# Optimization experiments

Hardware: AMD Instinct MI355X
Metric: run time of the kernel (lower is better)

## Reference

```python
import jax, jax.numpy as jnp
import numpy as np

EMB = 1024
FF = 4096
NE = 8
TOPK = 2
TEMP = 1.0


def setup_inputs() -> dict:
    key = jax.random.key(0)
    ks = jax.random.split(key, 8)
    s_emb = 1.0 / np.sqrt(EMB)
    s_ff = 1.0 / np.sqrt(FF)
    x = jax.random.normal(ks[0], (4, 2048, EMB), dtype=jnp.float32)
    gate_W = jax.random.uniform(ks[1], (EMB, NE), minval=-s_emb, maxval=s_emb, dtype=jnp.float32)
    gate_b = jax.random.uniform(ks[2], (NE,), minval=-s_emb, maxval=s_emb, dtype=jnp.float32)
    W1 = jax.random.uniform(ks[3], (NE, EMB, FF), minval=-s_emb, maxval=s_emb, dtype=jnp.float32)
    b1 = jax.random.uniform(ks[4], (NE, FF), minval=-s_emb, maxval=s_emb, dtype=jnp.float32)
    W2 = jax.random.uniform(ks[5], (NE, FF, EMB), minval=-s_ff, maxval=s_ff, dtype=jnp.float32)
    b2 = jax.random.uniform(ks[6], (NE, EMB), minval=-s_ff, maxval=s_ff, dtype=jnp.float32)
    return {"x": x, "gate_W": gate_W, "gate_b": gate_b, "W1": W1, "b1": b1, "W2": W2, "b2": b2}


def reference(x, gate_W, gate_b, W1, b1, W2, b2):
    B, S, D = x.shape
    xf = x.reshape(-1, D)  # [T, D]
    T = xf.shape[0]

    gate_logits = (xf @ gate_W + gate_b) / TEMP            # [T, E]
    gate_scores = jax.nn.softmax(gate_logits, axis=-1)     # [T, E]
    topk_scores, topk_idx = jax.lax.top_k(gate_scores, TOPK)
    topk_scores = topk_scores / jnp.sum(topk_scores, axis=-1, keepdims=True)

    # combine_weights[t, e] = sum_i topk_scores[t, i] * (topk_idx[t, i] == e)
    onehot = jax.nn.one_hot(topk_idx, NE, dtype=xf.dtype)  # [T, K, E]
    combine = jnp.einsum('tk,tke->te', topk_scores, onehot)  # [T, E]

    # Dense per-expert FFN (dropout is identity in eval): h = gelu(x W1 + b1); y = h W2 + b2
    h = jax.nn.gelu(jnp.einsum('td,edf->etf', xf, W1) + b1[:, None, :], approximate=False)
    y = jnp.einsum('etf,efd->etd', h, W2) + b2[:, None, :]  # [E, T, D]
    out = jnp.einsum('te,etd->td', combine, y).reshape(B, S, D)

    # Load-balance auxiliary loss
    expert_counts = jnp.sum(onehot, axis=(0, 1))            # [E]
    expert_fraction = expert_counts / (T * TOPK)
    routing_weights = jnp.mean(gate_scores, axis=0)
    aux_loss = NE * jnp.sum(expert_fraction * routing_weights)
    return out, aux_loss
```

## Files before the change

### kernel.cpp

```cpp
#include <hip/hip_runtime.h>
#include <math.h>

#define EMB 1024
#define FF  4096
#define NE  8
#define TTOK 8192

typedef __attribute__((ext_vector_type(4))) float  f32x4;
typedef __attribute__((ext_vector_type(8))) __bf16 bf16x8;
typedef __attribute__((ext_vector_type(4))) __bf16 bf16x4;

#define MAXROWS  18432

#define WS_COUNTS  0
#define WS_CURSORS 1024
#define WS_SSUM    1056
#define WS_NTILES  2080
#define WS_BASE    2084
#define WS_TILE_E  2176
#define WS_TILE_RB 2816
#define WS_TKIDX   4096
#define WS_TKW     69632
#define WS_SLOT    135168
#define WS_TOKID   200704
#define WS_ROWW    274432
#define WS_BIG2    350208

#define SZ_W1T ((size_t)NE * EMB * FF * 2)
#define SZ_W2T ((size_t)NE * EMB * FF * 2)
#define SZ_XB  ((size_t)TTOK * EMB * 2)
#define SZ_H   ((size_t)MAXROWS * FF * 2)
#define SZ_XG  ((size_t)MAXROWS * EMB * 2)
#define SZ_Y2  ((size_t)MAXROWS * EMB * 2)

__device__ inline f32x4 fzero() { f32x4 v = {0.f, 0.f, 0.f, 0.f}; return v; }

__device__ __forceinline__ void gl16(const void* g, void* l) {
    __builtin_amdgcn_global_load_lds(
        (const __attribute__((address_space(1))) void*)g,
        (__attribute__((address_space(3))) void*)l, 16, 0, 0);
}

#define DSR(dst, addr, off) \
    asm volatile("ds_read_b128 %0, %1 offset:" #off : "=v"(dst) : "v"(addr))

__device__ __forceinline__ float gelu_f(float v) {
    float u = fabsf(v) * 0.70710678118654752f;
    float p = 1.0f + u * (0.278393f + u * (0.230389f + u * (0.000972f + u * 0.078108f)));
    p = p * p; p = p * p;
    float er = 1.0f - 1.0f / p;
    float s = (v >= 0.0f) ? er : -er;
    return 0.5f * v * (1.0f + s);
}

__global__ __launch_bounds__(256) void gate_kernel(
    const float* __restrict__ x, const float* __restrict__ gW, const float* __restrict__ gb,
    int* counts, float* ssum, int* tk_idx, float* tk_w, __bf16* __restrict__ xb)
{
    int wave = threadIdx.x >> 6;
    int lane = threadIdx.x & 63;
    int t = blockIdx.x * 4 + wave;

    float acc[NE];
#pragma unroll
    for (int e = 0; e < NE; e++) acc[e] = 0.f;

    const float* xr = x + (size_t)t * EMB;
    __bf16* xbr = xb + (size_t)t * EMB;
#pragma unroll
    for (int i = 0; i < 4; i++) {
        int d0 = i * 256 + lane * 4;
        f32x4 xv = *(const f32x4*)(xr + d0);
        bf16x4 cv;
#pragma unroll
        for (int q = 0; q < 4; q++) cv[q] = (__bf16)xv[q];
        *(bf16x4*)(xbr + d0) = cv;
#pragma unroll
        for (int j = 0; j < 4; j++) {
            const float* wrow = gW + (size_t)(d0 + j) * NE;
            float xs = xv[j];
#pragma unroll
            for (int e = 0; e < NE; e++) acc[e] += xs * wrow[e];
        }
    }
#pragma unroll
    for (int e = 0; e < NE; e++) {
#pragma unroll
        for (int off = 32; off; off >>= 1) acc[e] += __shfl_xor(acc[e], off, 64);
    }
    if (lane == 0) {
        float sc[NE];
        float m = -1e30f;
        for (int e = 0; e < NE; e++) { sc[e] = acc[e] + gb[e]; m = fmaxf(m, sc[e]); }
        float sum = 0.f;
        for (int e = 0; e < NE; e++) { sc[e] = expf(sc[e] - m); sum += sc[e]; }
        float inv = 1.f / sum;
        for (int e = 0; e < NE; e++) sc[e] *= inv;
        int i0 = 0; float s0 = sc[0];
        for (int e = 1; e < NE; e++) if (sc[e] > s0) { s0 = sc[e]; i0 = e; }
        int i1 = -1; float s1 = -1e30f;
        for (int e = 0; e < NE; e++) if (e != i0 && sc[e] > s1) { s1 = sc[e]; i1 = e; }
        float rn = 1.f / (s0 + s1);
        tk_idx[2 * t]     = i0;  tk_idx[2 * t + 1] = i1;
        tk_w[2 * t]       = s0 * rn;  tk_w[2 * t + 1] = s1 * rn;
        int slot = blockIdx.x & 31;
        atomicAdd(&counts[i0 * 32 + slot], 1);
        atomicAdd(&counts[i1 * 32 + slot], 1);
        for (int e = 0; e < NE; e++) atomicAdd(&ssum[e * 32 + slot], sc[e]);
    }
}

__global__ void route_build_kernel(const int* counts, const float* ssum,
                                   int* ntiles, int* base, int* tile_e, int* tile_rb,
                                   float* out_aux)
{
    if (threadIdx.x != 0 || blockIdx.x != 0) return;
    int total = 0, tiles = 0;
    float aux = 0.f;
    for (int e = 0; e < NE; e++) {
        int c = 0; float ss = 0.f;
        for (int j = 0; j < 32; j++) { c += counts[e * 32 + j]; ss += ssum[e * 32 + j]; }
        base[e] = total;
        int nt = (c + 255) >> 8;
        for (int i = 0; i < nt; i++) { tile_e[tiles] = e; tile_rb[tiles] = total + (i << 8); tiles++; }
        total += nt << 8;
        aux += ((float)c / (float)(TTOK * 2)) * (ss / (float)TTOK);
    }
    *ntiles = tiles;
    *out_aux = aux * (float)NE;
}

__global__ __launch_bounds__(256) void scatter_kernel(
    const int* __restrict__ tk_idx, const float* __restrict__ tk_w,
    const int* __restrict__ base, int* cursors, int* token_id, float* roww,
    int* slot_of)
{
    int t = blockIdx.x * 256 + threadIdx.x;
#pragma unroll
    for (int k = 0; k < 2; k++) {
        int e = tk_idx[2 * t + k];
        int pos = atomicAdd(&cursors[e], 1);
        int slot = base[e] + pos;
        token_id[slot] = t;
        roww[slot] = tk_w[2 * t + k];
        slot_of[2 * t + k] = slot;
    }
}

__global__ __launch_bounds__(256) void pack_x_kernel(
    const __bf16* __restrict__ xb, const int* __restrict__ token_id,
    __bf16* __restrict__ xg)
{
    int tid = threadIdx.x;
    int slot = blockIdx.x * 2 + (tid >> 7);
    int off = (tid & 127) * 8;
    int tok = token_id[slot];
    uint4 v = {0u, 0u, 0u, 0u};
    if (tok >= 0) v = *(const uint4*)(xb + (size_t)tok * EMB + off);
    *(uint4*)(xg + (size_t)slot * EMB + off) = v;
}

__global__ __launch_bounds__(256) void combine_kernel(
    const __bf16* __restrict__ y0, const __bf16* __restrict__ y1, int nsplit,
    const int* __restrict__ slot_of,
    const int* __restrict__ tk_idx, const float* __restrict__ tk_w,
    const float* __restrict__ b2, float* __restrict__ out)
{
    int t = blockIdx.x;
    int dq = threadIdx.x * 4;
    int s0 = slot_of[2 * t], s1 = slot_of[2 * t + 1];
    int e0 = tk_idx[2 * t], e1 = tk_idx[2 * t + 1];
    float w0 = tk_w[2 * t], w1 = tk_w[2 * t + 1];
    bf16x4 va = *(const bf16x4*)(y0 + (size_t)s0 * EMB + dq);
    bf16x4 vb = *(const bf16x4*)(y0 + (size_t)s1 * EMB + dq);
    f32x4 ya, yb;
#pragma unroll
    for (int q = 0; q < 4; q++) { ya[q] = (float)va[q]; yb[q] = (float)vb[q]; }
    if (nsplit == 2) {
        bf16x4 za = *(const bf16x4*)(y1 + (size_t)s0 * EMB + dq);
        bf16x4 zb = *(const bf16x4*)(y1 + (size_t)s1 * EMB + dq);
#pragma unroll
        for (int q = 0; q < 4; q++) { ya[q] += (float)za[q]; yb[q] += (float)zb[q]; }
    }
    f32x4 ba = *(const f32x4*)(b2 + (size_t)e0 * EMB + dq);
    f32x4 bb = *(const f32x4*)(b2 + (size_t)e1 * EMB + dq);
    f32x4 r;
#pragma unroll
    for (int q = 0; q < 4; q++) r[q] = w0 * (ya[q] + ba[q]) + w1 * (yb[q] + bb[q]);
    *(f32x4*)(out + (size_t)t * EMB + dq) = r;
}

__global__ __launch_bounds__(256) void transpose_cvt2_kernel(
    const float* __restrict__ W1, __bf16* __restrict__ W1T,
    const float* __restrict__ W2, __bf16* __restrict__ W2T)
{
    int f = blockIdx.x;
    int which = f >> 13; f &= 8191;
    int e = f >> 10; f &= 1023;
    int R, C, bx, by;
    const float* src; __bf16* dst;
    if (which == 0) { R = EMB; C = FF;  bx = f & 15; by = f >> 4; src = W1; dst = W1T; }
    else            { R = FF;  C = EMB; bx = f & 63; by = f >> 6; src = W2; dst = W2T; }
    src += (size_t)e * R * C;
    dst += (size_t)e * R * C;
    __shared__ __bf16 Ls[64 * 72];
    int t = threadIdx.x;
    int r0 = bx * 64, c0 = by * 64;
    int ri = t >> 4, cj = (t & 15) * 4;
#pragma unroll
    for (int p = 0; p < 4; p++) {
        int r = ri + p * 16;
        f32x4 v = *(const f32x4*)(src + (size_t)(r0 + r) * C + c0 + cj);
#pragma unroll
        for (int q = 0; q < 4; q++) Ls[(cj + q) * 72 + r] = (__bf16)v[q];
    }
    __syncthreads();
    int c = t >> 2, rq = (t & 3) * 16;
    bf16x8 a = *(bf16x8*)&Ls[c * 72 + rq];
    bf16x8 b = *(bf16x8*)&Ls[c * 72 + rq + 8];
    *(bf16x8*)(dst + (size_t)(c0 + c) * R + r0 + rq) = a;
    *(bf16x8*)(dst + (size_t)(c0 + c) * R + r0 + rq + 8) = b;
}


template <bool PACKED>
__global__ __launch_bounds__(512, 2) void gemm1_8p(
    const __bf16* __restrict__ xsrc, const __bf16* __restrict__ W1T,
    const float* __restrict__ b1,
    const int* __restrict__ token_id, const int* __restrict__ tile_e,
    const int* __restrict__ tile_rb, const int* __restrict__ ntiles,
    __bf16* __restrict__ h)
{
    extern __shared__ __bf16 lds[];
    int flat = blockIdx.x;
    int c8 = flat & 7, r = flat >> 3;
    int mti = r >> 4, nb = r & 15;
    int mt = c8 * 9 + mti;
    if (mt >= *ntiles) return;
    int e = tile_e[mt], rb = tile_rb[mt];
    int n0 = nb * 256;

    int tid = threadIdx.x, lane = tid & 63, wid = tid >> 6;
    int wr = wid >> 2, wc = wid & 3;
    int cl = lane & 15, cq = lane >> 4;

    int srow = tid >> 2;
    int schunk = (tid & 3) ^ ((tid >> 3) & 3);
    const __bf16* ag[2];
#pragma unroll
    for (int hm = 0; hm < 2; hm++) {
        if (PACKED) {
            ag[hm] = xsrc + (size_t)(rb + hm * 128 + srow) * EMB + schunk * 8;
        } else {
            int tok = token_id[rb + hm * 128 + srow];
            if (tok < 0) tok = 0;
            ag[hm] = xsrc + (size_t)tok * EMB + schunk * 8;
        }
    }
    const __bf16* bg[2];
#pragma unroll
    for (int hn = 0; hn < 2; hn++)
        bg[hn] = W1T + ((size_t)e * FF + (size_t)(n0 + hn * 128 + srow)) * EMB + schunk * 8;

    int sdA0 = wid * 512, sdA1 = 4096 + wid * 512;
    int sdB0 = 8192 + wid * 512, sdB1 = 12288 + wid * 512;

    uint32_t lb = (uint32_t)(uintptr_t)(__attribute__((address_space(3))) __bf16*)lds;
    int xoffe = (cq ^ ((cl >> 1) & 3)) * 8;
    uint32_t ab0 = lb + 2u * (uint32_t)(wr * 4096 + cl * 32 + xoffe);
    uint32_t bb0 = lb + 2u * (uint32_t)(8192 + (wc >> 1) * 4096 + ((wc & 1) * 64 + cl) * 32 + xoffe);

    f32x4 acc[8][4];
#pragma unroll
    for (int i = 0; i < 8; i++)
#pragma unroll
        for (int j = 0; j < 4; j++) acc[i][j] = fzero();

    const int NT = EMB / 32;
#pragma unroll
    for (int t0 = 0; t0 < 3; t0++) {
        __bf16* bp = lds + t0 * 16384;
        int k0 = t0 * 32;
        gl16(ag[0] + k0, bp + sdA0);
        gl16(ag[1] + k0, bp + sdA1);
        gl16(bg[0] + k0, bp + sdB0);
        gl16(bg[1] + k0, bp + sdB1);
    }
    asm volatile("s_waitcnt vmcnt(8)" ::: "memory");
    __builtin_amdgcn_s_barrier();

#pragma unroll 1
    for (int t = 0; t < NT; t++) {
        uint32_t cboff = (uint32_t)(t & 3) * 32768u;
        uint32_t aaddr = ab0 + cboff, baddr = bb0 + cboff;
        bf16x8 b[4], a[8];
        DSR(b[0], baddr, 0);    DSR(b[1], baddr, 1024);
        DSR(b[2], baddr, 2048); DSR(b[3], baddr, 3072);
        DSR(a[0], aaddr, 0);    DSR(a[1], aaddr, 1024);
        DSR(a[2], aaddr, 2048); DSR(a[3], aaddr, 3072);
        DSR(a[4], aaddr, 4096); DSR(a[5], aaddr, 5120);
        DSR(a[6], aaddr, 6144); DSR(a[7], aaddr, 7168);

        int kt = t + 3;
        if (kt < NT) {
            __bf16* sp = lds + (kt & 3) * 16384;
            int ko = kt * 32;
            gl16(ag[0] + ko, sp + sdA0);
            gl16(ag[1] + ko, sp + sdA1);
            gl16(bg[0] + ko, sp + sdB0);
            gl16(bg[1] + ko, sp + sdB1);
        }

        asm volatile("s_waitcnt lgkmcnt(0)" ::: "memory");
        __builtin_amdgcn_sched_barrier(0);
        __builtin_amdgcn_s_setprio(1);
#pragma unroll
        for (int mi = 0; mi < 8; mi++)
#pragma unroll
            for (int ni = 0; ni < 4; ni++)
                acc[mi][ni] = __builtin_amdgcn_mfma_f32_16x16x32_bf16(a[mi], b[ni], acc[mi][ni], 0, 0, 0);
        __builtin_amdgcn_s_setprio(0);

        if (t < NT - 3)       { asm volatile("s_waitcnt vmcnt(8)" ::: "memory"); }
        else if (t == NT - 3) { asm volatile("s_waitcnt vmcnt(4)" ::: "memory"); }
        else if (t == NT - 2) { asm volatile("s_waitcnt vmcnt(0)" ::: "memory"); }
        if (t < NT - 1) __builtin_amdgcn_s_barrier();
    }

    const float* b1g = b1 + (size_t)e * FF + n0;
#pragma unroll
    for (int mi = 0; mi < 8; mi++) {
#pragma unroll
        for (int ni = 0; ni < 4; ni++) {
            int col = wc * 64 + ni * 16 + cl;
            float bias = b1g[col];
#pragma unroll
            for (int j = 0; j < 4; j++) {
                int row = wr * 128 + mi * 16 + cq * 4 + j;
                float v = acc[mi][ni][j] + bias;
                h[(size_t)(rb + row) * FF + n0 + col] = (__bf16)gelu_f(v);
            }
        }
    }
}

__global__ __launch_bounds__(512, 2) void gemm2_8p(
    const __bf16* __restrict__ h, const __bf16* __restrict__ W2T,
    const int* __restrict__ tile_e, const int* __restrict__ tile_rb,
    const int* __restrict__ ntiles,
    __bf16* __restrict__ y0, __bf16* __restrict__ y1, int nsplit)
{
    extern __shared__ __bf16 lds[];
    int flat = blockIdx.x;
    int c8 = flat & 7, r = flat >> 3;
    int z = r / 36; int r36 = r - z * 36;
    int mti = r36 >> 2, nb = r36 & 3;
    int mt = c8 * 9 + mti;
    if (mt >= *ntiles) return;
    int e = tile_e[mt], rb = tile_rb[mt];
    int n0 = nb * 256;
    int KC = FF / nsplit;
    int koff = z * KC;
    __bf16* y = z ? y1 : y0;

    int tid = threadIdx.x, lane = tid & 63, wid = tid >> 6;
    int wr = wid >> 2, wc = wid & 3;
    int cl = lane & 15, cq = lane >> 4;

    int srow = tid >> 2;
    int schunk = (tid & 3) ^ ((tid >> 3) & 3);
    const __bf16* ag[2];
#pragma unroll
    for (int hm = 0; hm < 2; hm++)
        ag[hm] = h + (size_t)(rb + hm * 128 + srow) * FF + koff + schunk * 8;
    const __bf16* bg[2];
#pragma unroll
    for (int hn = 0; hn < 2; hn++)
        bg[hn] = W2T + ((size_t)e * EMB + (size_t)(n0 + hn * 128 + srow)) * FF + koff + schunk * 8;

    int sdA0 = wid * 512, sdA1 = 4096 + wid * 512;
    int sdB0 = 8192 + wid * 512, sdB1 = 12288 + wid * 512;

    uint32_t lb = (uint32_t)(uintptr_t)(__attribute__((address_space(3))) __bf16*)lds;
    int xoffe = (cq ^ ((cl >> 1) & 3)) * 8;
    uint32_t ab0 = lb + 2u * (uint32_t)(wr * 4096 + cl * 32 + xoffe);
    uint32_t bb0 = lb + 2u * (uint32_t)(8192 + (wc >> 1) * 4096 + ((wc & 1) * 64 + cl) * 32 + xoffe);

    f32x4 acc[8][4];
#pragma unroll
    for (int i = 0; i < 8; i++)
#pragma unroll
        for (int j = 0; j < 4; j++) acc[i][j] = fzero();

    const int NT = KC / 32;
#pragma unroll
    for (int t0 = 0; t0 < 3; t0++) {
        __bf16* bp = lds + t0 * 16384;
        int k0 = t0 * 32;
        gl16(ag[0] + k0, bp + sdA0);
        gl16(ag[1] + k0, bp + sdA1);
        gl16(bg[0] + k0, bp + sdB0);
        gl16(bg[1] + k0, bp + sdB1);
    }
    asm volatile("s_waitcnt vmcnt(8)" ::: "memory");
    __builtin_amdgcn_s_barrier();

#pragma unroll 1
    for (int t = 0; t < NT; t++) {
        uint32_t cboff = (uint32_t)(t & 3) * 32768u;
        uint32_t aaddr = ab0 + cboff, baddr = bb0 + cboff;
        bf16x8 b[4], a[8];
        DSR(b[0], baddr, 0);    DSR(b[1], baddr, 1024);
        DSR(b[2], baddr, 2048); DSR(b[3], baddr, 3072);
        DSR(a[0], aaddr, 0);    DSR(a[1], aaddr, 1024);
        DSR(a[2], aaddr, 2048); DSR(a[3], aaddr, 3072);
        DSR(a[4], aaddr, 4096); DSR(a[5], aaddr, 5120);
        DSR(a[6], aaddr, 6144); DSR(a[7], aaddr, 7168);

        int kt = t + 3;
        if (kt < NT) {
            __bf16* sp = lds + (kt & 3) * 16384;
            int ko = kt * 32;
            gl16(ag[0] + ko, sp + sdA0);
            gl16(ag[1] + ko, sp + sdA1);
            gl16(bg[0] + ko, sp + sdB0);
            gl16(bg[1] + ko, sp + sdB1);
        }

        asm volatile("s_waitcnt lgkmcnt(0)" ::: "memory");
        __builtin_amdgcn_sched_barrier(0);
        __builtin_amdgcn_s_setprio(1);
#pragma unroll
        for (int mi = 0; mi < 8; mi++)
#pragma unroll
            for (int ni = 0; ni < 4; ni++)
                acc[mi][ni] = __builtin_amdgcn_mfma_f32_16x16x32_bf16(a[mi], b[ni], acc[mi][ni], 0, 0, 0);
        __builtin_amdgcn_s_setprio(0);

        if (t < NT - 3)       { asm volatile("s_waitcnt vmcnt(8)" ::: "memory"); }
        else if (t == NT - 3) { asm volatile("s_waitcnt vmcnt(4)" ::: "memory"); }
        else if (t == NT - 2) { asm volatile("s_waitcnt vmcnt(0)" ::: "memory"); }
        if (t < NT - 1) __builtin_amdgcn_s_barrier();
    }

#pragma unroll
    for (int mi = 0; mi < 8; mi++) {
#pragma unroll
        for (int ni = 0; ni < 4; ni++) {
            int col = wc * 64 + ni * 16 + cl;
#pragma unroll
            for (int j = 0; j < 4; j++) {
                int row = wr * 128 + mi * 16 + cq * 4 + j;
                y[(size_t)(rb + row) * EMB + n0 + col] = (__bf16)acc[mi][ni][j];
            }
        }
    }
}

extern "C" void kernel_launch(void* const* d_in, const int* in_sizes, int n_in,
                              void* d_out, int out_size, void* d_ws, size_t ws_size,
                              hipStream_t stream)
{
    const float* x   = (const float*)d_in[0];
    const float* gW  = (const float*)d_in[1];
    const float* gb  = (const float*)d_in[2];
    const float* W1  = (const float*)d_in[3];
    const float* b1  = (const float*)d_in[4];
    const float* W2  = (const float*)d_in[5];
    const float* b2  = (const float*)d_in[6];
    float* out = (float*)d_out;

    char* ws = (char*)d_ws;
    int*   counts  = (int*)(ws + WS_COUNTS);
    int*   cursors = (int*)(ws + WS_CURSORS);
    float* ssum    = (float*)(ws + WS_SSUM);
    int*   ntiles  = (int*)(ws + WS_NTILES);
    int*   base    = (int*)(ws + WS_BASE);
    int*   tile_e  = (int*)(ws + WS_TILE_E);
    int*   tile_rb = (int*)(ws + WS_TILE_RB);
    int*   tk_idx  = (int*)(ws + WS_TKIDX);
    float* tk_w    = (float*)(ws + WS_TKW);
    int*   slot_of = (int*)(ws + WS_SLOT);
    int*   token_id= (int*)(ws + WS_TOKID);
    float* roww    = (float*)(ws + WS_ROWW);

    __bf16* W1T  = (__bf16*)(ws + WS_BIG2);
    __bf16* xb   = (__bf16*)(ws + WS_BIG2 + SZ_W1T);
    __bf16* W2T  = (__bf16*)(ws + WS_BIG2 + SZ_W1T + SZ_XB);
    __bf16* hbuf = (__bf16*)(ws + WS_BIG2 + SZ_W1T + SZ_XB + SZ_W2T);
    size_t fixedend = WS_BIG2 + SZ_W1T + SZ_XB + SZ_W2T;

    __bf16* y0 = (__bf16*)(ws + WS_BIG2);
    __bf16* xg = (__bf16*)(ws + fixedend + SZ_H);
    bool packed = (ws_size >= fixedend + SZ_H + SZ_XG);
    __bf16* y1 = (__bf16*)(ws + fixedend + SZ_H + (packed ? SZ_XG : 0));
    int nsplit = (ws_size >= fixedend + SZ_H + (packed ? SZ_XG : 0) + SZ_Y2) ? 2 : 1;

    hipFuncSetAttribute((const void*)gemm1_8p<true>,  hipFuncAttributeMaxDynamicSharedMemorySize, 131072);
    hipFuncSetAttribute((const void*)gemm1_8p<false>, hipFuncAttributeMaxDynamicSharedMemorySize, 131072);
    hipFuncSetAttribute((const void*)gemm2_8p, hipFuncAttributeMaxDynamicSharedMemorySize, 131072);

    hipMemsetAsync(ws + WS_COUNTS, 0, 2080, stream);
    hipMemsetAsync(ws + WS_TOKID, 0xFF, (size_t)MAXROWS * 4, stream);

    transpose_cvt2_kernel<<<16384, 256, 0, stream>>>(W1, W1T, W2, W2T);

    gate_kernel<<<TTOK / 4, 256, 0, stream>>>(x, gW, gb, counts, ssum, tk_idx, tk_w, xb);
    route_build_kernel<<<1, 64, 0, stream>>>(counts, ssum, ntiles, base, tile_e, tile_rb,
                                             out + (size_t)TTOK * EMB);
    scatter_kernel<<<TTOK / 256, 256, 0, stream>>>(tk_idx, tk_w, base, cursors, token_id, roww, slot_of);

    if (packed) {
        pack_x_kernel<<<MAXROWS / 2, 256, 0, stream>>>(xb, token_id, xg);
        gemm1_8p<true><<<8 * 9 * 16, 512, 131072, stream>>>(
            xg, W1T, b1, token_id, tile_e, tile_rb, ntiles, hbuf);
    } else {
        gemm1_8p<false><<<8 * 9 * 16, 512, 131072, stream>>>(
            xb, W1T, b1, token_id, tile_e, tile_rb, ntiles, hbuf);
    }
    gemm2_8p<<<8 * 9 * 4 * nsplit, 512, 131072, stream>>>(
        hbuf, W2T, tile_e, tile_rb, ntiles, y0, y1, nsplit);
    combine_kernel<<<TTOK, 256, 0, stream>>>(y0, y1, nsplit, slot_of, tk_idx, tk_w, b2, out);
}
```

Before: 685.5 us.

## Shrink expert GEMM tiles to 128x128 with 256 threads and triple buffering

Both grouped expert GEMMs move from 256x256 output tiles (512 threads, 4-stage LDS ring, 128KB) to 128x128 tiles (256 threads, 3-stage ring, 48KB), with three blocks per CU. The grid grows fourfold, which improves load balance and wave filling across the CUs and gives more resident blocks to hide latency. In exchange, each block reuses its operands less, so global and L2 traffic per FLOP roughly doubles, and the prefetch depth drops from three stages to two.

```diff
diff --git a/kernel.cpp b/kernel.cpp
--- a/kernel.cpp
+++ b/kernel.cpp
@@ -224,7 +224,7 @@
 
 
 template <bool PACKED>
-__global__ __launch_bounds__(512, 2) void gemm1_8p(
+__global__ __launch_bounds__(256, 3) void gemm1_8p(
     const __bf16* __restrict__ xsrc, const __bf16* __restrict__ W1T,
     const float* __restrict__ b1,
     const int* __restrict__ token_id, const int* __restrict__ tile_e,
@@ -234,25 +234,27 @@
     extern __shared__ __bf16 lds[];
     int flat = blockIdx.x;
     int c8 = flat & 7, r = flat >> 3;
-    int mti = r >> 4, nb = r & 15;
-    int mt = c8 * 9 + mti;
-    if (mt >= *ntiles) return;
-    int e = tile_e[mt], rb = tile_rb[mt];
-    int n0 = nb * 256;
+    int sti = r >> 5, nb = r & 31;
+    int st = c8 * 18 + sti;
+    if (st >= *ntiles * 2) return;
+    int e = tile_e[st >> 1];
+    int rb = tile_rb[st >> 1] + (st & 1) * 128;
+    int n0 = nb * 128;
 
     int tid = threadIdx.x, lane = tid & 63, wid = tid >> 6;
-    int wr = wid >> 2, wc = wid & 3;
+    int wr = wid >> 1, wc = wid & 1;
     int cl = lane & 15, cq = lane >> 4;
 
-    int srow = tid >> 2;
+    int srow1 = ((tid >> 6) << 4) | ((tid & 63) >> 2);
     int schunk = (tid & 3) ^ ((tid >> 3) & 3);
     const __bf16* ag[2];
 #pragma unroll
     for (int hm = 0; hm < 2; hm++) {
+        int row = srow1 + hm * 64;
         if (PACKED) {
-            ag[hm] = xsrc + (size_t)(rb + hm * 128 + srow) * EMB + schunk * 8;
+            ag[hm] = xsrc + (size_t)(rb + row) * EMB + schunk * 8;
         } else {
-            int tok = token_id[rb + hm * 128 + srow];
+            int tok = token_id[rb + row];
             if (tok < 0) tok = 0;
             ag[hm] = xsrc + (size_t)tok * EMB + schunk * 8;
         }
@@ -260,50 +262,50 @@
     const __bf16* bg[2];
 #pragma unroll
     for (int hn = 0; hn < 2; hn++)
-        bg[hn] = W1T + ((size_t)e * FF + (size_t)(n0 + hn * 128 + srow)) * EMB + schunk * 8;
-
-    int sdA0 = wid * 512, sdA1 = 4096 + wid * 512;
-    int sdB0 = 8192 + wid * 512, sdB1 = 12288 + wid * 512;
+        bg[hn] = W1T + ((size_t)e * FF + (size_t)(n0 + srow1 + hn * 64)) * EMB + schunk * 8;
+
+    int sdA0 = wid * 512, sdA1 = 2048 + wid * 512;
+    int sdB0 = 4096 + wid * 512, sdB1 = 6144 + wid * 512;
 
     uint32_t lb = (uint32_t)(uintptr_t)(__attribute__((address_space(3))) __bf16*)lds;
     int xoffe = (cq ^ ((cl >> 1) & 3)) * 8;
-    uint32_t ab0 = lb + 2u * (uint32_t)(wr * 4096 + cl * 32 + xoffe);
-    uint32_t bb0 = lb + 2u * (uint32_t)(8192 + (wc >> 1) * 4096 + ((wc & 1) * 64 + cl) * 32 + xoffe);
-
-    f32x4 acc[8][4];
-#pragma unroll
-    for (int i = 0; i < 8; i++)
+    uint32_t ab0 = lb + 2u * (uint32_t)(wr * 2048 + cl * 32 + xoffe);
+    uint32_t bb0 = lb + 2u * (uint32_t)(4096 + wc * 2048 + cl * 32 + xoffe);
+
+    f32x4 acc[4][4];
+#pragma unroll
+    for (int i = 0; i < 4; i++)
 #pragma unroll
         for (int j = 0; j < 4; j++) acc[i][j] = fzero();
 
     const int NT = EMB / 32;
 #pragma unroll
-    for (int t0 = 0; t0 < 3; t0++) {
-        __bf16* bp = lds + t0 * 16384;
+    for (int t0 = 0; t0 < 2; t0++) {
+        __bf16* bp = lds + t0 * 8192;
         int k0 = t0 * 32;
         gl16(ag[0] + k0, bp + sdA0);
         gl16(ag[1] + k0, bp + sdA1);
         gl16(bg[0] + k0, bp + sdB0);
         gl16(bg[1] + k0, bp + sdB1);
     }
-    asm volatile("s_waitcnt vmcnt(8)" ::: "memory");
+    asm volatile("s_waitcnt vmcnt(4)" ::: "memory");
     __builtin_amdgcn_s_barrier();
 
+    int cb = 0;
 #pragma unroll 1
     for (int t = 0; t < NT; t++) {
-        uint32_t cboff = (uint32_t)(t & 3) * 32768u;
+        uint32_t cboff = (uint32_t)cb * 16384u;
         uint32_t aaddr = ab0 + cboff, baddr = bb0 + cboff;
-        bf16x8 b[4], a[8];
+        bf16x8 b[4], a[4];
         DSR(b[0], baddr, 0);    DSR(b[1], baddr, 1024);
         DSR(b[2], baddr, 2048); DSR(b[3], baddr, 3072);
         DSR(a[0], aaddr, 0);    DSR(a[1], aaddr, 1024);
         DSR(a[2], aaddr, 2048); DSR(a[3], aaddr, 3072);
-        DSR(a[4], aaddr, 4096); DSR(a[5], aaddr, 5120);
-        DSR(a[6], aaddr, 6144); DSR(a[7], aaddr, 7168);
-
-        int kt = t + 3;
+
+        int kt = t + 2;
         if (kt < NT) {
-            __bf16* sp = lds + (kt & 3) * 16384;
+            int sb = cb + 2; if (sb >= 3) sb -= 3;
+            __bf16* sp = lds + sb * 8192;
             int ko = kt * 32;
             gl16(ag[0] + ko, sp + sdA0);
             gl16(ag[1] + ko, sp + sdA1);
@@ -315,28 +317,28 @@
         __builtin_amdgcn_sched_barrier(0);
         __builtin_amdgcn_s_setprio(1);
 #pragma unroll
-        for (int mi = 0; mi < 8; mi++)
+        for (int mi = 0; mi < 4; mi++)
 #pragma unroll
             for (int ni = 0; ni < 4; ni++)
                 acc[mi][ni] = __builtin_amdgcn_mfma_f32_16x16x32_bf16(a[mi], b[ni], acc[mi][ni], 0, 0, 0);
         __builtin_amdgcn_s_setprio(0);
 
-        if (t < NT - 3)       { asm volatile("s_waitcnt vmcnt(8)" ::: "memory"); }
-        else if (t == NT - 3) { asm volatile("s_waitcnt vmcnt(4)" ::: "memory"); }
+        if (t < NT - 2)       { asm volatile("s_waitcnt vmcnt(4)" ::: "memory"); }
         else if (t == NT - 2) { asm volatile("s_waitcnt vmcnt(0)" ::: "memory"); }
         if (t < NT - 1) __builtin_amdgcn_s_barrier();
+        cb = cb + 1; if (cb >= 3) cb = 0;
     }
 
     const float* b1g = b1 + (size_t)e * FF + n0;
 #pragma unroll
-    for (int mi = 0; mi < 8; mi++) {
+    for (int mi = 0; mi < 4; mi++) {
 #pragma unroll
         for (int ni = 0; ni < 4; ni++) {
             int col = wc * 64 + ni * 16 + cl;
             float bias = b1g[col];
 #pragma unroll
             for (int j = 0; j < 4; j++) {
-                int row = wr * 128 + mi * 16 + cq * 4 + j;
+                int row = wr * 64 + mi * 16 + cq * 4 + j;
                 float v = acc[mi][ni][j] + bias;
                 h[(size_t)(rb + row) * FF + n0 + col] = (__bf16)gelu_f(v);
             }
@@ -344,7 +346,7 @@
     }
 }
 
-__global__ __launch_bounds__(512, 2) void gemm2_8p(
+__global__ __launch_bounds__(256, 3) void gemm2_8p(
     const __bf16* __restrict__ h, const __bf16* __restrict__ W2T,
     const int* __restrict__ tile_e, const int* __restrict__ tile_rb,
     const int* __restrict__ ntiles,
@@ -353,73 +355,74 @@
     extern __shared__ __bf16 lds[];
     int flat = blockIdx.x;
     int c8 = flat & 7, r = flat >> 3;
-    int z = r / 36; int r36 = r - z * 36;
-    int mti = r36 >> 2, nb = r36 & 3;
-    int mt = c8 * 9 + mti;
-    if (mt >= *ntiles) return;
-    int e = tile_e[mt], rb = tile_rb[mt];
-    int n0 = nb * 256;
+    int z = r / 144; int r144 = r - z * 144;
+    int sti = r144 >> 3, nb = r144 & 7;
+    int st = c8 * 18 + sti;
+    if (st >= *ntiles * 2) return;
+    int e = tile_e[st >> 1];
+    int rb = tile_rb[st >> 1] + (st & 1) * 128;
+    int n0 = nb * 128;
     int KC = FF / nsplit;
     int koff = z * KC;
     __bf16* y = z ? y1 : y0;
 
     int tid = threadIdx.x, lane = tid & 63, wid = tid >> 6;
-    int wr = wid >> 2, wc = wid & 3;
+    int wr = wid >> 1, wc = wid & 1;
     int cl = lane & 15, cq = lane >> 4;
 
-    int srow = tid >> 2;
+    int srow1 = ((tid >> 6) << 4) | ((tid & 63) >> 2);
     int schunk = (tid & 3) ^ ((tid >> 3) & 3);
     const __bf16* ag[2];
 #pragma unroll
     for (int hm = 0; hm < 2; hm++)
-        ag[hm] = h + (size_t)(rb + hm * 128 + srow) * FF + koff + schunk * 8;
+        ag[hm] = h + (size_t)(rb + srow1 + hm * 64) * FF + koff + schunk * 8;
     const __bf16* bg[2];
 #pragma unroll
     for (int hn = 0; hn < 2; hn++)
-        bg[hn] = W2T + ((size_t)e * EMB + (size_t)(n0 + hn * 128 + srow)) * FF + koff + schunk * 8;
-
-    int sdA0 = wid * 512, sdA1 = 4096 + wid * 512;
-    int sdB0 = 8192 + wid * 512, sdB1 = 12288 + wid * 512;
+        bg[hn] = W2T + ((size_t)e * EMB + (size_t)(n0 + srow1 + hn * 64)) * FF + koff + schunk * 8;
+
+    int sdA0 = wid * 512, sdA1 = 2048 + wid * 512;
+    int sdB0 = 4096 + wid * 512, sdB1 = 6144 + wid * 512;
 
     uint32_t lb = (uint32_t)(uintptr_t)(__attribute__((address_space(3))) __bf16*)lds;
     int xoffe = (cq ^ ((cl >> 1) & 3)) * 8;
-    uint32_t ab0 = lb + 2u * (uint32_t)(wr * 4096 + cl * 32 + xoffe);
-    uint32_t bb0 = lb + 2u * (uint32_t)(8192 + (wc >> 1) * 4096 + ((wc & 1) * 64 + cl) * 32 + xoffe);
-
-    f32x4 acc[8][4];
-#pragma unroll
-    for (int i = 0; i < 8; i++)
+    uint32_t ab0 = lb + 2u * (uint32_t)(wr * 2048 + cl * 32 + xoffe);
+    uint32_t bb0 = lb + 2u * (uint32_t)(4096 + wc * 2048 + cl * 32 + xoffe);
+
+    f32x4 acc[4][4];
+#pragma unroll
+    for (int i = 0; i < 4; i++)
 #pragma unroll
         for (int j = 0; j < 4; j++) acc[i][j] = fzero();
 
     const int NT = KC / 32;
 #pragma unroll
-    for (int t0 = 0; t0 < 3; t0++) {
-        __bf16* bp = lds + t0 * 16384;
+    for (int t0 = 0; t0 < 2; t0++) {
+        __bf16* bp = lds + t0 * 8192;
         int k0 = t0 * 32;
         gl16(ag[0] + k0, bp + sdA0);
         gl16(ag[1] + k0, bp + sdA1);
         gl16(bg[0] + k0, bp + sdB0);
         gl16(bg[1] + k0, bp + sdB1);
     }
-    asm volatile("s_waitcnt vmcnt(8)" ::: "memory");
+    asm volatile("s_waitcnt vmcnt(4)" ::: "memory");
     __builtin_amdgcn_s_barrier();
 
+    int cb = 0;
 #pragma unroll 1
     for (int t = 0; t < NT; t++) {
-        uint32_t cboff = (uint32_t)(t & 3) * 32768u;
+        uint32_t cboff = (uint32_t)cb * 16384u;
         uint32_t aaddr = ab0 + cboff, baddr = bb0 + cboff;
-        bf16x8 b[4], a[8];
+        bf16x8 b[4], a[4];
         DSR(b[0], baddr, 0);    DSR(b[1], baddr, 1024);
         DSR(b[2], baddr, 2048); DSR(b[3], baddr, 3072);
         DSR(a[0], aaddr, 0);    DSR(a[1], aaddr, 1024);
         DSR(a[2], aaddr, 2048); DSR(a[3], aaddr, 3072);
-        DSR(a[4], aaddr, 4096); DSR(a[5], aaddr, 5120);
-        DSR(a[6], aaddr, 6144); DSR(a[7], aaddr, 7168);
-
-        int kt = t + 3;
+
+        int kt = t + 2;
         if (kt < NT) {
-            __bf16* sp = lds + (kt & 3) * 16384;
+            int sb = cb + 2; if (sb >= 3) sb -= 3;
+            __bf16* sp = lds + sb * 8192;
             int ko = kt * 32;
             gl16(ag[0] + ko, sp + sdA0);
             gl16(ag[1] + ko, sp + sdA1);
@@ -431,26 +434,26 @@
         __builtin_amdgcn_sched_barrier(0);
         __builtin_amdgcn_s_setprio(1);
 #pragma unroll
-        for (int mi = 0; mi < 8; mi++)
+        for (int mi = 0; mi < 4; mi++)
 #pragma unroll
             for (int ni = 0; ni < 4; ni++)
                 acc[mi][ni] = __builtin_amdgcn_mfma_f32_16x16x32_bf16(a[mi], b[ni], acc[mi][ni], 0, 0, 0);
         __builtin_amdgcn_s_setprio(0);
 
-        if (t < NT - 3)       { asm volatile("s_waitcnt vmcnt(8)" ::: "memory"); }
-        else if (t == NT - 3) { asm volatile("s_waitcnt vmcnt(4)" ::: "memory"); }
+        if (t < NT - 2)       { asm volatile("s_waitcnt vmcnt(4)" ::: "memory"); }
         else if (t == NT - 2) { asm volatile("s_waitcnt vmcnt(0)" ::: "memory"); }
         if (t < NT - 1) __builtin_amdgcn_s_barrier();
-    }
-
-#pragma unroll
-    for (int mi = 0; mi < 8; mi++) {
+        cb = cb + 1; if (cb >= 3) cb = 0;
+    }
+
+#pragma unroll
+    for (int mi = 0; mi < 4; mi++) {
 #pragma unroll
         for (int ni = 0; ni < 4; ni++) {
             int col = wc * 64 + ni * 16 + cl;
 #pragma unroll
             for (int j = 0; j < 4; j++) {
-                int row = wr * 128 + mi * 16 + cq * 4 + j;
+                int row = wr * 64 + mi * 16 + cq * 4 + j;
                 y[(size_t)(rb + row) * EMB + n0 + col] = (__bf16)acc[mi][ni][j];
             }
         }
@@ -496,9 +499,9 @@
     __bf16* y1 = (__bf16*)(ws + fixedend + SZ_H + (packed ? SZ_XG : 0));
     int nsplit = (ws_size >= fixedend + SZ_H + (packed ? SZ_XG : 0) + SZ_Y2) ? 2 : 1;
 
-    hipFuncSetAttribute((const void*)gemm1_8p<true>,  hipFuncAttributeMaxDynamicSharedMemorySize, 131072);
-    hipFuncSetAttribute((const void*)gemm1_8p<false>, hipFuncAttributeMaxDynamicSharedMemorySize, 131072);
-    hipFuncSetAttribute((const void*)gemm2_8p, hipFuncAttributeMaxDynamicSharedMemorySize, 131072);
+    hipFuncSetAttribute((const void*)gemm1_8p<true>,  hipFuncAttributeMaxDynamicSharedMemorySize, 49152);
+    hipFuncSetAttribute((const void*)gemm1_8p<false>, hipFuncAttributeMaxDynamicSharedMemorySize, 49152);
+    hipFuncSetAttribute((const void*)gemm2_8p, hipFuncAttributeMaxDynamicSharedMemorySize, 49152);
 
     hipMemsetAsync(ws + WS_COUNTS, 0, 2080, stream);
     hipMemsetAsync(ws + WS_TOKID, 0xFF, (size_t)MAXROWS * 4, stream);
@@ -512,13 +515,13 @@
 
     if (packed) {
         pack_x_kernel<<<MAXROWS / 2, 256, 0, stream>>>(xb, token_id, xg);
-        gemm1_8p<true><<<8 * 9 * 16, 512, 131072, stream>>>(
+        gemm1_8p<true><<<8 * 18 * 32, 256, 49152, stream>>>(
             xg, W1T, b1, token_id, tile_e, tile_rb, ntiles, hbuf);
     } else {
-        gemm1_8p<false><<<8 * 9 * 16, 512, 131072, stream>>>(
+        gemm1_8p<false><<<8 * 18 * 32, 256, 49152, stream>>>(
             xb, W1T, b1, token_id, tile_e, tile_rb, ntiles, hbuf);
     }
-    gemm2_8p<<<8 * 9 * 4 * nsplit, 512, 131072, stream>>>(
+    gemm2_8p<<<8 * 18 * 8 * nsplit, 256, 49152, stream>>>(
         hbuf, W2T, tile_e, tile_rb, ntiles, y0, y1, nsplit);
     combine_kernel<<<TTOK, 256, 0, stream>>>(y0, y1, nsplit, slot_of, tk_idx, tk_w, b2, out);
 }
```

Result: no change. 687.4 us (+0.3%).
